# Performance work log

Measured on AMD Instinct MI355X. Metric: run time of the kernel, lower is better.

The kernel has to match this reference:

```python
import jax, jax.numpy as jnp
import numpy as np

L, NH, H, V, MAXP = 12, 12, 768, 50257, 1024
HD = H // NH
EPS = 1e-5


def setup_inputs() -> dict:
    key = jax.random.key(0)
    ks = iter(jax.random.split(key, 32))
    s = 0.02
    inp = {
        "input_ids": jax.random.randint(next(ks), (8, 1024), 0, V),
        "tok_emb": jax.random.normal(next(ks), (V, H), jnp.float32) * s,
        "pos_emb": jax.random.normal(next(ks), (MAXP, H), jnp.float32) * s,
        "ln1_g": jnp.ones((L, H), jnp.float32),
        "ln1_b": jnp.zeros((L, H), jnp.float32),
        "w_attn": jax.random.normal(next(ks), (L, H, 3 * H), jnp.float32) * s,
        "b_attn": jnp.zeros((L, 3 * H), jnp.float32),
        "w_out": jax.random.normal(next(ks), (L, H, H), jnp.float32) * s,
        "b_out": jnp.zeros((L, H), jnp.float32),
        "ln2_g": jnp.ones((L, H), jnp.float32),
        "ln2_b": jnp.zeros((L, H), jnp.float32),
        "w1": jax.random.normal(next(ks), (L, H, 4 * H), jnp.float32) * s,
        "b1": jnp.zeros((L, 4 * H), jnp.float32),
        "w2": jax.random.normal(next(ks), (L, 4 * H, H), jnp.float32) * s,
        "b2": jnp.zeros((L, H), jnp.float32),
        "lnf_g": jnp.ones((H,), jnp.float32),
        "lnf_b": jnp.zeros((H,), jnp.float32),
    }
    return inp


def _ln(x, g, b):
    mu = jnp.mean(x, axis=-1, keepdims=True)
    var = jnp.var(x, axis=-1, keepdims=True)
    return (x - mu) * jax.lax.rsqrt(var + EPS) * g + b


def _gpt2_forward(input_ids, tok_emb, pos_emb, ln1_g, ln1_b, w_attn, b_attn,
                  w_out, b_out, ln2_g, ln2_b, w1, b1, w2, b2, lnf_g, lnf_b):
    B, S = input_ids.shape
    x = tok_emb[input_ids] + pos_emb[:S]  # [B,S,H]
    # causal mask: True above the diagonal (future positions)
    mask = jnp.triu(jnp.ones((S, S), dtype=bool), k=1)
    inv_sqrt_hd = 1.0 / np.sqrt(HD)
    for l in range(L):
        n1 = _ln(x, ln1_g[l], ln1_b[l])
        qkv = n1 @ w_attn[l] + b_attn[l]  # [B,S,3H]
        q, k, v = jnp.split(qkv, 3, axis=-1)
        q = q.reshape(B, S, NH, HD).transpose(0, 2, 1, 3)
        k = k.reshape(B, S, NH, HD).transpose(0, 2, 1, 3)
        v = v.reshape(B, S, NH, HD).transpose(0, 2, 1, 3)
        scores = jnp.einsum('bhtd,bhsd->bhts', q, k)  # [B,NH,S,S]
        # faithful to source: mask with -10000 BEFORE dividing by sqrt(head_size)
        scores = jnp.where(mask, -10000.0, scores) * inv_sqrt_hd
        probs = jax.nn.softmax(scores, axis=-1)
        attn = jnp.einsum('bhts,bhsd->bhtd', probs, v)
        attn = attn.transpose(0, 2, 1, 3).reshape(B, S, H)
        attn = attn @ w_out[l] + b_out[l]
        x = x + attn
        n2 = _ln(x, ln2_g[l], ln2_b[l])
        h = jax.nn.gelu(n2 @ w1[l] + b1[l], approximate=False)
        x = x + (h @ w2[l] + b2[l])
    x = _ln(x, lnf_g, lnf_b)
    final_encoding = x[:, -1]  # [B,H]
    logits = final_encoding @ tok_emb.T  # tied weights, [B,V]
    return logits, final_encoding


def reference(input_ids, tok_emb, pos_emb, ln1_g, ln1_b, w_attn, b_attn,
              w_out, b_out, ln2_g, ln2_b, w1, b1, w2, b2, lnf_g, lnf_b):
    return _gpt2_forward(input_ids, tok_emb, pos_emb, ln1_g, ln1_b, w_attn,
                         b_attn, w_out, b_out, ln2_g, ln2_b, w1, b1, w2, b2,
                         lnf_g, lnf_b)
```

## Files before the change

kernel.cpp:

```cpp
#include <hip/hip_runtime.h>
#include <cmath>

typedef unsigned short u16;
typedef __bf16 bf16;
typedef __attribute__((ext_vector_type(8))) bf16 bf16x8;
typedef __attribute__((ext_vector_type(4))) float f32x4;

#define DINL __device__ __forceinline__

#define BB 8
#define SS 1024
#define HH 768
#define LL 12
#define NHH 12
#define HDD 64
#define MM 8192
#define VV 50257

DINL u16 f2bf(float f) {
    unsigned int u = __builtin_bit_cast(unsigned int, f);
    u += 0x7fff + ((u >> 16) & 1);
    return (u16)(u >> 16);
}

DINL bf16x8 ld_bf8(const u16* p) { return *(const bf16x8*)p; }

typedef __attribute__((address_space(1))) unsigned int as1_u32;
typedef __attribute__((address_space(3))) unsigned int as3_u32;

DINL void gllds16(const void* g, void* l) {
    __builtin_amdgcn_global_load_lds((as1_u32*)g, (as3_u32*)l, 16, 0, 0);
}

DINL void xcd_remap(int gx, int& mTile, int& nTile) {
    int i = blockIdx.y * gx + blockIdx.x;
    int xcd = i & 7, j = i >> 3;
    nTile = j % gx;
    mTile = (j / gx) * 8 + xcd;
}

__global__ __launch_bounds__(256) void k_embed(const int* __restrict__ ids,
                                               const float* __restrict__ tok,
                                               const float* __restrict__ pos,
                                               float* __restrict__ x) {
    int tk = blockIdx.x;
    int s = tk & (SS - 1);
    int id = ids[tk];
    const float* tr = tok + (size_t)id * HH;
    const float* pr = pos + (size_t)s * HH;
    float* xr = x + (size_t)tk * HH;
#pragma unroll
    for (int j = 0; j < 3; j++) {
        int d = threadIdx.x + j * 256;
        xr[d] = tr[d] + pr[d];
    }
}

__global__ __launch_bounds__(256) void k_tcvt(const float* __restrict__ src, u16* __restrict__ dst,
                                              int R, int C, size_t sstr, size_t dstr) {
    src += (size_t)blockIdx.z * sstr;
    dst += (size_t)blockIdx.z * dstr;
    __shared__ float t[32][33];
    int tx = threadIdx.x & 31, ty = threadIdx.x >> 5;
    int c0 = blockIdx.x * 32, r0 = blockIdx.y * 32;
#pragma unroll
    for (int p = 0; p < 4; p++)
        t[ty + p * 8][tx] = src[(size_t)(r0 + ty + p * 8) * C + c0 + tx];
    __syncthreads();
#pragma unroll
    for (int p = 0; p < 4; p++)
        dst[(size_t)(c0 + ty + p * 8) * R + r0 + tx] = f2bf(t[tx][ty + p * 8]);
}

template <bool F32OUT>
__global__ __launch_bounds__(256) void k_ln(const float* __restrict__ x, const float* __restrict__ g,
                                            const float* __restrict__ b, void* __restrict__ outp,
                                            int nrows, int rs, int ro) {
    int w = threadIdx.x >> 6, lane = threadIdx.x & 63;
    int row = blockIdx.x * 4 + w;
    if (row >= nrows) return;
    const float4* xr = (const float4*)(x + ((size_t)row * rs + ro) * HH);
    float4 v[3];
    float s = 0.f, s2 = 0.f;
#pragma unroll
    for (int j = 0; j < 3; j++) {
        v[j] = xr[lane + 64 * j];
        s += v[j].x + v[j].y + v[j].z + v[j].w;
        s2 += v[j].x * v[j].x + v[j].y * v[j].y + v[j].z * v[j].z + v[j].w * v[j].w;
    }
#pragma unroll
    for (int off = 32; off; off >>= 1) {
        s += __shfl_xor(s, off, 64);
        s2 += __shfl_xor(s2, off, 64);
    }
    float mu = s * (1.0f / HH);
    float rstd = rsqrtf(s2 * (1.0f / HH) - mu * mu + 1e-5f);
#pragma unroll
    for (int j = 0; j < 3; j++) {
        int d4 = lane + 64 * j;
        float4 gv = ((const float4*)g)[d4];
        float4 bv = ((const float4*)b)[d4];
        float o0 = (v[j].x - mu) * rstd * gv.x + bv.x;
        float o1 = (v[j].y - mu) * rstd * gv.y + bv.y;
        float o2 = (v[j].z - mu) * rstd * gv.z + bv.z;
        float o3 = (v[j].w - mu) * rstd * gv.w + bv.w;
        if (F32OUT) {
            ((float4*)outp)[(size_t)row * (HH / 4) + d4] = make_float4(o0, o1, o2, o3);
        } else {
            ushort4 pk;
            pk.x = f2bf(o0); pk.y = f2bf(o1); pk.z = f2bf(o2); pk.w = f2bf(o3);
            *(ushort4*)((u16*)outp + (size_t)row * HH + d4 * 4) = pk;
        }
    }
}

template <int EPI>
__global__ __launch_bounds__(256) void k_gemm(const u16* __restrict__ A, const u16* __restrict__ BT,
                                              const float* __restrict__ bias, float* __restrict__ xio,
                                              u16* __restrict__ obuf, u16* __restrict__ qb,
                                              u16* __restrict__ kb, u16* __restrict__ vb,
                                              int N, int K) {
    __shared__ u16 As[2][128 * 32];
    __shared__ u16 Bs[2][128 * 32];
    const int t = threadIdx.x, w = t >> 6, lane = t & 63;
    const int l15 = lane & 15, l4 = lane >> 4;
    const int wr = w >> 1, wc = w & 1;
    int mT, nT;
    xcd_remap(gridDim.x, mT, nT);
    const int m0 = mT * 128, n0 = nT * 128;
    const int KT = K >> 5;

    f32x4 acc[4][4] = {};

    auto stage = [&](int buf, int kt) {
#pragma unroll
        for (int i = 0; i < 2; i++) {
            int idx = w * 2 + i;
            int row = idx * 16 + (lane >> 2);
            int kc = kt * 32 + (((lane & 3) ^ ((lane >> 3) & 3)) * 8);
            gllds16(A + (size_t)(m0 + row) * K + kc, &As[buf][idx * 512]);
            gllds16(BT + (size_t)(n0 + row) * K + kc, &Bs[buf][idx * 512]);
        }
    };

    stage(0, 0);
    __syncthreads();
    int buf = 0;
    const int sw = (l15 >> 1) & 3;
    for (int kt = 0; kt < KT; ++kt) {
        if (kt + 1 < KT) stage(buf ^ 1, kt + 1);
        bf16x8 af[4], bfr[4];
#pragma unroll
        for (int i = 0; i < 4; i++) af[i] = ld_bf8(&As[buf][(wr * 64 + i * 16 + l15) * 32 + ((l4 ^ sw) * 8)]);
#pragma unroll
        for (int j = 0; j < 4; j++) bfr[j] = ld_bf8(&Bs[buf][(wc * 64 + j * 16 + l15) * 32 + ((l4 ^ sw) * 8)]);
#pragma unroll
        for (int i = 0; i < 4; i++)
#pragma unroll
            for (int j = 0; j < 4; j++)
                acc[i][j] = __builtin_amdgcn_mfma_f32_16x16x32_bf16(af[i], bfr[j], acc[i][j], 0, 0, 0);
        __syncthreads();
        buf ^= 1;
    }

#pragma unroll
    for (int i = 0; i < 4; i++) {
#pragma unroll
        for (int j = 0; j < 4; j++) {
#pragma unroll
            for (int r = 0; r < 4; r++) {
                int row = m0 + wr * 64 + i * 16 + l4 * 4 + r;
                int n = n0 + wc * 64 + j * 16 + l15;
                float v = acc[i][j][r] + bias[n];
                if (EPI == 0) {
                    int seg = n / HH, wi = n % HH;
                    int h = wi >> 6, d = wi & 63;
                    int bi = row >> 10, s = row & (SS - 1);
                    size_t bh = (size_t)(bi * NHH + h);
                    if (seg == 0)
                        qb[(bh * SS + s) * HDD + d] = f2bf(v);
                    else if (seg == 1)
                        kb[(bh * SS + s) * HDD + d] = f2bf(v);
                    else
                        vb[(bh * HDD + d) * SS + s] = f2bf(v);
                } else if (EPI == 1) {
                    xio[(size_t)row * N + n] += v;
                } else {
                    float gl = 0.5f * v * (1.0f + erff(v * 0.70710678118654752f));
                    obuf[(size_t)row * N + n] = f2bf(gl);
                }
            }
        }
    }
}

__global__ __launch_bounds__(256) void k_gemm64(const u16* __restrict__ A, const u16* __restrict__ BT,
                                                const float* __restrict__ bias, float* __restrict__ xio,
                                                int N, int K) {
    __shared__ u16 As[2][128 * 32];
    __shared__ u16 Bs[2][64 * 32];
    const int t = threadIdx.x, w = t >> 6, lane = t & 63;
    const int l15 = lane & 15, l4 = lane >> 4;
    const int wr = w >> 1, wc = w & 1;
    int mT, nT;
    xcd_remap(gridDim.x, mT, nT);
    const int m0 = mT * 128, n0 = nT * 64;
    const int KT = K >> 5;

    f32x4 acc[4][2] = {};

    auto stage = [&](int buf, int kt) {
        int rr = lane >> 2;
        int kc = kt * 32 + (((lane & 3) ^ ((lane >> 3) & 3)) * 8);
#pragma unroll
        for (int i = 0; i < 2; i++) {
            int idx = w * 2 + i;
            gllds16(A + (size_t)(m0 + idx * 16 + rr) * K + kc, &As[buf][idx * 512]);
        }
        gllds16(BT + (size_t)(n0 + w * 16 + rr) * K + kc, &Bs[buf][w * 512]);
    };

    stage(0, 0);
    __syncthreads();
    int buf = 0;
    const int sw = (l15 >> 1) & 3;
    for (int kt = 0; kt < KT; ++kt) {
        if (kt + 1 < KT) stage(buf ^ 1, kt + 1);
        bf16x8 af[4], bfr[2];
#pragma unroll
        for (int i = 0; i < 4; i++) af[i] = ld_bf8(&As[buf][(wr * 64 + i * 16 + l15) * 32 + ((l4 ^ sw) * 8)]);
#pragma unroll
        for (int j = 0; j < 2; j++) bfr[j] = ld_bf8(&Bs[buf][(wc * 32 + j * 16 + l15) * 32 + ((l4 ^ sw) * 8)]);
#pragma unroll
        for (int i = 0; i < 4; i++)
#pragma unroll
            for (int j = 0; j < 2; j++)
                acc[i][j] = __builtin_amdgcn_mfma_f32_16x16x32_bf16(af[i], bfr[j], acc[i][j], 0, 0, 0);
        __syncthreads();
        buf ^= 1;
    }

#pragma unroll
    for (int i = 0; i < 4; i++) {
#pragma unroll
        for (int j = 0; j < 2; j++) {
#pragma unroll
            for (int r = 0; r < 4; r++) {
                int row = m0 + wr * 64 + i * 16 + l4 * 4 + r;
                int n = n0 + wc * 32 + j * 16 + l15;
                xio[(size_t)row * N + n] += acc[i][j][r] + bias[n];
            }
        }
    }
}

__global__ __launch_bounds__(256) void k_attn(const u16* __restrict__ q, const u16* __restrict__ k,
                                              const u16* __restrict__ vt, u16* __restrict__ o) {
    int qt = 15 - blockIdx.x;
    int bh = blockIdx.y;
    int w = threadIdx.x >> 6, lane = threadIdx.x & 63;
    int l15 = lane & 15, l4 = lane >> 4;

    __shared__ u16 Ks[2][64 * 64];
    __shared__ u16 Vs[2][64 * 64];
    __shared__ u16 pl[4][16 * 72];
    u16* pw = pl[w];

    const size_t bhq = (size_t)bh * SS * HDD;
    int qrow0 = qt * 64 + w * 16;

    auto stage = [&](int buf, int kvb) {
#pragma unroll
        for (int i = 0; i < 2; i++) {
            int rl = w * 16 + i * 8 + (lane >> 3);
            int c = lane & 7;
            int sc = (c ^ (rl & 7)) * 8;
            gllds16(k + bhq + (size_t)(kvb * 64 + rl) * HDD + sc, &Ks[buf][(w * 16 + i * 8) * 64]);
            gllds16(vt + ((size_t)bh * HDD + rl) * SS + kvb * 64 + sc, &Vs[buf][(w * 16 + i * 8) * 64]);
        }
    };

    bf16x8 aq[2];
#pragma unroll
    for (int ks = 0; ks < 2; ks++)
        aq[ks] = ld_bf8(q + bhq + (size_t)(qrow0 + l15) * HDD + ks * 32 + l4 * 8);

    f32x4 acc[4] = {};
    float mrun[4], psum[4];
#pragma unroll
    for (int r = 0; r < 4; r++) { mrun[r] = -1e30f; psum[r] = 0.f; }

    stage(0, 0);
    __syncthreads();
    int buf = 0;

    for (int kvb = 0; kvb <= qt; ++kvb) {
        if (kvb < qt) stage(buf ^ 1, kvb + 1);

        f32x4 s[4] = {};
#pragma unroll
        for (int c = 0; c < 4; c++) {
#pragma unroll
            for (int ks = 0; ks < 2; ks++) {
                bf16x8 kf = ld_bf8(&Ks[buf][(c * 16 + l15) * 64 + ((ks * 4 + l4) ^ (l15 & 7)) * 8]);
                s[c] = __builtin_amdgcn_mfma_f32_16x16x32_bf16(aq[ks], kf, s[c], 0, 0, 0);
            }
        }
        bool diag = (kvb == qt);
#pragma unroll
        for (int c = 0; c < 4; c++) {
#pragma unroll
            for (int r = 0; r < 4; r++) {
                float val = s[c][r] * 0.125f;
                if (diag) {
                    int kvi = kvb * 64 + c * 16 + l15;
                    int qi = qrow0 + l4 * 4 + r;
                    if (kvi > qi) val = -1250.0f;
                }
                s[c][r] = val;
            }
        }
        float lmax[4];
#pragma unroll
        for (int r = 0; r < 4; r++)
            lmax[r] = fmaxf(fmaxf(s[0][r], s[1][r]), fmaxf(s[2][r], s[3][r]));
        int ok = 1;
#pragma unroll
        for (int r = 0; r < 4; r++) ok &= (lmax[r] <= mrun[r] + 8.f) ? 1 : 0;
        if (!__all(ok)) {
#pragma unroll
            for (int off = 1; off < 16; off <<= 1)
#pragma unroll
                for (int r = 0; r < 4; r++) lmax[r] = fmaxf(lmax[r], __shfl_xor(lmax[r], off, 64));
#pragma unroll
            for (int r = 0; r < 4; r++) {
                float mnew = fmaxf(mrun[r], lmax[r]);
                float ef = __expf(mrun[r] - mnew);
                mrun[r] = mnew;
                psum[r] *= ef;
#pragma unroll
                for (int cd = 0; cd < 4; cd++) acc[cd][r] *= ef;
            }
        }
#pragma unroll
        for (int c = 0; c < 4; c++)
#pragma unroll
            for (int r = 0; r < 4; r++) {
                float pv = __expf(s[c][r] - mrun[r]);
                psum[r] += pv;
                pw[(l4 * 4 + r) * 72 + c * 16 + l15] = f2bf(pv);
            }
#pragma unroll
        for (int ks = 0; ks < 2; ks++) {
            bf16x8 pa = ld_bf8(pw + l15 * 72 + ks * 32 + l4 * 8);
#pragma unroll
            for (int cd = 0; cd < 4; cd++) {
                bf16x8 vf = ld_bf8(&Vs[buf][(cd * 16 + l15) * 64 + ((ks * 4 + l4) ^ (l15 & 7)) * 8]);
                acc[cd] = __builtin_amdgcn_mfma_f32_16x16x32_bf16(pa, vf, acc[cd], 0, 0, 0);
            }
        }
        __syncthreads();
        buf ^= 1;
    }

#pragma unroll
    for (int off = 1; off < 16; off <<= 1)
#pragma unroll
        for (int r = 0; r < 4; r++) psum[r] += __shfl_xor(psum[r], off, 64);

    int b = bh / NHH, h = bh % NHH;
#pragma unroll
    for (int cd = 0; cd < 4; cd++) {
#pragma unroll
        for (int r = 0; r < 4; r++) {
            int qi = qrow0 + l4 * 4 + r;
            float ov = acc[cd][r] / psum[r];
            o[((size_t)b * SS + qi) * HH + h * HDD + cd * 16 + l15] = f2bf(ov);
        }
    }
}

__global__ __launch_bounds__(256) void k_logits(const float* __restrict__ enc,
                                                const float* __restrict__ tok,
                                                float* __restrict__ out) {
    int w = threadIdx.x >> 6, lane = threadIdx.x & 63;
    int v = blockIdx.x * 4 + w;
    if (v >= VV) return;
    const float4* tr = (const float4*)(tok + (size_t)v * HH);
    float a[8];
#pragma unroll
    for (int b = 0; b < 8; b++) a[b] = 0.f;
#pragma unroll
    for (int j = 0; j < 3; j++) {
        float4 t4 = tr[lane + 64 * j];
#pragma unroll
        for (int b = 0; b < 8; b++) {
            float4 e4 = *(const float4*)(enc + (size_t)b * HH + (lane + 64 * j) * 4);
            a[b] += t4.x * e4.x + t4.y * e4.y + t4.z * e4.z + t4.w * e4.w;
        }
    }
#pragma unroll
    for (int off = 32; off; off >>= 1)
#pragma unroll
        for (int b = 0; b < 8; b++) a[b] += __shfl_xor(a[b], off, 64);
    if (lane == 0) {
#pragma unroll
        for (int b = 0; b < 8; b++) out[(size_t)b * VV + v] = a[b];
    }
}

extern "C" void kernel_launch(void* const* d_in, const int* in_sizes, int n_in,
                              void* d_out, int out_size, void* d_ws, size_t ws_size,
                              hipStream_t stream) {
    const int* ids = (const int*)d_in[0];
    const float* tok = (const float*)d_in[1];
    const float* pos = (const float*)d_in[2];
    const float* ln1g = (const float*)d_in[3];
    const float* ln1b = (const float*)d_in[4];
    const float* wat = (const float*)d_in[5];
    const float* bat = (const float*)d_in[6];
    const float* wou = (const float*)d_in[7];
    const float* bou = (const float*)d_in[8];
    const float* ln2g = (const float*)d_in[9];
    const float* ln2b = (const float*)d_in[10];
    const float* w1 = (const float*)d_in[11];
    const float* b1 = (const float*)d_in[12];
    const float* w2 = (const float*)d_in[13];
    const float* b2 = (const float*)d_in[14];
    const float* lnfg = (const float*)d_in[15];
    const float* lnfb = (const float*)d_in[16];

    char* ws = (char*)d_ws;
    float* xw = (float*)(ws + 0);
    u16* nb = (u16*)(ws + 25165824);
    u16* qb = (u16*)(ws + 37748736);
    u16* kb = (u16*)(ws + 50331648);
    u16* vb = (u16*)(ws + 62914560);
    u16* ab = (u16*)(ws + 75497472);
    u16* hb = (u16*)(ws + 88080384);
    u16* wt = (u16*)(ws + 138412032);
    const size_t LSTR = 7077888;
    const size_t WAO = 0, WOO = 1769472, W1O = 2359296, W2O = 4718592;

    float* outf = (float*)d_out;
    float* enc = outf + (size_t)BB * VV;

    k_embed<<<MM, 256, 0, stream>>>(ids, tok, pos, xw);
    k_tcvt<<<dim3(72, 24, 12), 256, 0, stream>>>(wat, wt + WAO, 768, 2304, (size_t)768 * 2304, LSTR);
    k_tcvt<<<dim3(24, 24, 12), 256, 0, stream>>>(wou, wt + WOO, 768, 768, (size_t)768 * 768, LSTR);
    k_tcvt<<<dim3(96, 24, 12), 256, 0, stream>>>(w1, wt + W1O, 768, 3072, (size_t)768 * 3072, LSTR);
    k_tcvt<<<dim3(24, 96, 12), 256, 0, stream>>>(w2, wt + W2O, 3072, 768, (size_t)3072 * 768, LSTR);

    for (int l = 0; l < LL; l++) {
        const u16* wl = wt + (size_t)l * LSTR;
        k_ln<false><<<MM / 4, 256, 0, stream>>>(xw, ln1g + l * HH, ln1b + l * HH, nb, MM, 1, 0);
        k_gemm<0><<<dim3(18, 64), 256, 0, stream>>>(nb, wl + WAO, bat + (size_t)l * 2304,
                                                    nullptr, nullptr, qb, kb, vb, 2304, 768);
        k_attn<<<dim3(16, 96), 256, 0, stream>>>(qb, kb, vb, ab);
        k_gemm64<<<dim3(12, 64), 256, 0, stream>>>(ab, wl + WOO, bou + (size_t)l * HH, xw, 768, 768);
        k_ln<false><<<MM / 4, 256, 0, stream>>>(xw, ln2g + l * HH, ln2b + l * HH, nb, MM, 1, 0);
        k_gemm<2><<<dim3(24, 64), 256, 0, stream>>>(nb, wl + W1O, b1 + (size_t)l * 3072,
                                                    nullptr, hb, nullptr, nullptr, nullptr, 3072, 768);
        k_gemm64<<<dim3(12, 64), 256, 0, stream>>>(hb, wl + W2O, b2 + (size_t)l * HH, xw, 768, 3072);
    }
    k_ln<true><<<2, 256, 0, stream>>>(xw, lnfg, lnfb, enc, BB, SS, SS - 1);
    k_logits<<<(VV + 3) / 4, 256, 0, stream>>>(enc, tok, outf);
}
```

Baseline: 3.899 ms.

## Enlarge attention query tile to 128 rows and fold softmax scale into Q

The attention kernel now processes 128 query rows per block (32 per wave, two MFMA row groups), so each staged K/V tile in shared memory feeds twice as many queries and the grid halves. Waves skip KV blocks beyond their own causal limit, and the 1/sqrt(head_dim) scale moves into the QKV GEMM epilogue so the per-score multiply goes away. In exchange there is higher register pressure and fewer blocks (768 vs 1536), which may reduce occupancy and worsen causal load imbalance. Scaling Q before the bf16 cast also slightly changes rounding.

```diff
diff --git a/kernel.cpp b/kernel.cpp
--- a/kernel.cpp
+++ b/kernel.cpp
@@ -178,7 +178,7 @@
                     int bi = row >> 10, s = row & (SS - 1);
                     size_t bh = (size_t)(bi * NHH + h);
                     if (seg == 0)
-                        qb[(bh * SS + s) * HDD + d] = f2bf(v);
+                        qb[(bh * SS + s) * HDD + d] = f2bf(v * 0.125f);
                     else if (seg == 1)
                         kb[(bh * SS + s) * HDD + d] = f2bf(v);
                     else
@@ -256,18 +256,20 @@
 
 __global__ __launch_bounds__(256) void k_attn(const u16* __restrict__ q, const u16* __restrict__ k,
                                               const u16* __restrict__ vt, u16* __restrict__ o) {
-    int qt = 15 - blockIdx.x;
+    int qt = 7 - blockIdx.x;
     int bh = blockIdx.y;
     int w = threadIdx.x >> 6, lane = threadIdx.x & 63;
     int l15 = lane & 15, l4 = lane >> 4;
 
     __shared__ u16 Ks[2][64 * 64];
     __shared__ u16 Vs[2][64 * 64];
-    __shared__ u16 pl[4][16 * 72];
+    __shared__ u16 pl[4][32 * 72];
     u16* pw = pl[w];
 
     const size_t bhq = (size_t)bh * SS * HDD;
-    int qrow0 = qt * 64 + w * 16;
+    const int qrow0 = qt * 128 + w * 32;
+    const int nfull = qrow0 >> 6;
+    const int kvmax = 2 * qt + 1;
 
     auto stage = [&](int buf, int kvb) {
 #pragma unroll
@@ -280,83 +282,104 @@
         }
     };
 
-    bf16x8 aq[2];
-#pragma unroll
-    for (int ks = 0; ks < 2; ks++)
-        aq[ks] = ld_bf8(q + bhq + (size_t)(qrow0 + l15) * HDD + ks * 32 + l4 * 8);
-
-    f32x4 acc[4] = {};
-    float mrun[4], psum[4];
-#pragma unroll
-    for (int r = 0; r < 4; r++) { mrun[r] = -1e30f; psum[r] = 0.f; }
+    bf16x8 aq[2][2];
+#pragma unroll
+    for (int m = 0; m < 2; m++)
+#pragma unroll
+        for (int ks = 0; ks < 2; ks++)
+            aq[m][ks] = ld_bf8(q + bhq + (size_t)(qrow0 + m * 16 + l15) * HDD + ks * 32 + l4 * 8);
+
+    f32x4 acc[2][4] = {};
+    float mrun[2][4], psum[2][4];
+#pragma unroll
+    for (int m = 0; m < 2; m++)
+#pragma unroll
+        for (int r = 0; r < 4; r++) { mrun[m][r] = -1e30f; psum[m][r] = 0.f; }
 
     stage(0, 0);
     __syncthreads();
     int buf = 0;
 
-    for (int kvb = 0; kvb <= qt; ++kvb) {
-        if (kvb < qt) stage(buf ^ 1, kvb + 1);
-
-        f32x4 s[4] = {};
-#pragma unroll
-        for (int c = 0; c < 4; c++) {
+    for (int kvb = 0; kvb <= kvmax; ++kvb) {
+        if (kvb < kvmax) stage(buf ^ 1, kvb + 1);
+
+        if (kvb <= nfull) {
+            f32x4 s[2][4] = {};
+#pragma unroll
+            for (int c = 0; c < 4; c++) {
+#pragma unroll
+                for (int ks = 0; ks < 2; ks++) {
+                    bf16x8 kf = ld_bf8(&Ks[buf][(c * 16 + l15) * 64 + ((ks * 4 + l4) ^ (l15 & 7)) * 8]);
+#pragma unroll
+                    for (int m = 0; m < 2; m++)
+                        s[m][c] = __builtin_amdgcn_mfma_f32_16x16x32_bf16(aq[m][ks], kf, s[m][c], 0, 0, 0);
+                }
+            }
+            if (kvb == nfull) {
+#pragma unroll
+                for (int c = 0; c < 4; c++) {
+                    int kvi = kvb * 64 + c * 16 + l15;
+#pragma unroll
+                    for (int m = 0; m < 2; m++)
+#pragma unroll
+                        for (int r = 0; r < 4; r++) {
+                            int qi = qrow0 + m * 16 + l4 * 4 + r;
+                            if (kvi > qi) s[m][c][r] = -1250.0f;
+                        }
+                }
+            }
+            float lmax[2][4];
+            int ok = 1;
+#pragma unroll
+            for (int m = 0; m < 2; m++)
+#pragma unroll
+                for (int r = 0; r < 4; r++) {
+                    lmax[m][r] = fmaxf(fmaxf(s[m][0][r], s[m][1][r]), fmaxf(s[m][2][r], s[m][3][r]));
+                    ok &= (lmax[m][r] <= mrun[m][r] + 8.f) ? 1 : 0;
+                }
+            if (!__all(ok)) {
+#pragma unroll
+                for (int off = 1; off < 16; off <<= 1)
+#pragma unroll
+                    for (int m = 0; m < 2; m++)
+#pragma unroll
+                        for (int r = 0; r < 4; r++)
+                            lmax[m][r] = fmaxf(lmax[m][r], __shfl_xor(lmax[m][r], off, 64));
+#pragma unroll
+                for (int m = 0; m < 2; m++)
+#pragma unroll
+                    for (int r = 0; r < 4; r++) {
+                        float mnew = fmaxf(mrun[m][r], lmax[m][r]);
+                        float ef = __expf(mrun[m][r] - mnew);
+                        mrun[m][r] = mnew;
+                        psum[m][r] *= ef;
+#pragma unroll
+                        for (int cd = 0; cd < 4; cd++) acc[m][cd][r] *= ef;
+                    }
+            }
+#pragma unroll
+            for (int c = 0; c < 4; c++)
+#pragma unroll
+                for (int m = 0; m < 2; m++)
+#pragma unroll
+                    for (int r = 0; r < 4; r++) {
+                        float pv = __expf(s[m][c][r] - mrun[m][r]);
+                        psum[m][r] += pv;
+                        pw[(m * 16 + l4 * 4 + r) * 72 + c * 16 + l15] = f2bf(pv);
+                    }
 #pragma unroll
             for (int ks = 0; ks < 2; ks++) {
-                bf16x8 kf = ld_bf8(&Ks[buf][(c * 16 + l15) * 64 + ((ks * 4 + l4) ^ (l15 & 7)) * 8]);
-                s[c] = __builtin_amdgcn_mfma_f32_16x16x32_bf16(aq[ks], kf, s[c], 0, 0, 0);
-            }
-        }
-        bool diag = (kvb == qt);
-#pragma unroll
-        for (int c = 0; c < 4; c++) {
-#pragma unroll
-            for (int r = 0; r < 4; r++) {
-                float val = s[c][r] * 0.125f;
-                if (diag) {
-                    int kvi = kvb * 64 + c * 16 + l15;
-                    int qi = qrow0 + l4 * 4 + r;
-                    if (kvi > qi) val = -1250.0f;
+                bf16x8 pa[2];
+#pragma unroll
+                for (int m = 0; m < 2; m++)
+                    pa[m] = ld_bf8(pw + (m * 16 + l15) * 72 + ks * 32 + l4 * 8);
+#pragma unroll
+                for (int cd = 0; cd < 4; cd++) {
+                    bf16x8 vf = ld_bf8(&Vs[buf][(cd * 16 + l15) * 64 + ((ks * 4 + l4) ^ (l15 & 7)) * 8]);
+#pragma unroll
+                    for (int m = 0; m < 2; m++)
+                        acc[m][cd] = __builtin_amdgcn_mfma_f32_16x16x32_bf16(pa[m], vf, acc[m][cd], 0, 0, 0);
                 }
-                s[c][r] = val;
-            }
-        }
-        float lmax[4];
-#pragma unroll
-        for (int r = 0; r < 4; r++)
-            lmax[r] = fmaxf(fmaxf(s[0][r], s[1][r]), fmaxf(s[2][r], s[3][r]));
-        int ok = 1;
-#pragma unroll
-        for (int r = 0; r < 4; r++) ok &= (lmax[r] <= mrun[r] + 8.f) ? 1 : 0;
-        if (!__all(ok)) {
-#pragma unroll
-            for (int off = 1; off < 16; off <<= 1)
-#pragma unroll
-                for (int r = 0; r < 4; r++) lmax[r] = fmaxf(lmax[r], __shfl_xor(lmax[r], off, 64));
-#pragma unroll
-            for (int r = 0; r < 4; r++) {
-                float mnew = fmaxf(mrun[r], lmax[r]);
-                float ef = __expf(mrun[r] - mnew);
-                mrun[r] = mnew;
-                psum[r] *= ef;
-#pragma unroll
-                for (int cd = 0; cd < 4; cd++) acc[cd][r] *= ef;
-            }
-        }
-#pragma unroll
-        for (int c = 0; c < 4; c++)
-#pragma unroll
-            for (int r = 0; r < 4; r++) {
-                float pv = __expf(s[c][r] - mrun[r]);
-                psum[r] += pv;
-                pw[(l4 * 4 + r) * 72 + c * 16 + l15] = f2bf(pv);
-            }
-#pragma unroll
-        for (int ks = 0; ks < 2; ks++) {
-            bf16x8 pa = ld_bf8(pw + l15 * 72 + ks * 32 + l4 * 8);
-#pragma unroll
-            for (int cd = 0; cd < 4; cd++) {
-                bf16x8 vf = ld_bf8(&Vs[buf][(cd * 16 + l15) * 64 + ((ks * 4 + l4) ^ (l15 & 7)) * 8]);
-                acc[cd] = __builtin_amdgcn_mfma_f32_16x16x32_bf16(pa, vf, acc[cd], 0, 0, 0);
             }
         }
         __syncthreads();
@@ -366,18 +389,22 @@
 #pragma unroll
     for (int off = 1; off < 16; off <<= 1)
 #pragma unroll
-        for (int r = 0; r < 4; r++) psum[r] += __shfl_xor(psum[r], off, 64);
+        for (int m = 0; m < 2; m++)
+#pragma unroll
+            for (int r = 0; r < 4; r++) psum[m][r] += __shfl_xor(psum[m][r], off, 64);
 
     int b = bh / NHH, h = bh % NHH;
 #pragma unroll
-    for (int cd = 0; cd < 4; cd++) {
-#pragma unroll
-        for (int r = 0; r < 4; r++) {
-            int qi = qrow0 + l4 * 4 + r;
-            float ov = acc[cd][r] / psum[r];
-            o[((size_t)b * SS + qi) * HH + h * HDD + cd * 16 + l15] = f2bf(ov);
-        }
-    }
+    for (int m = 0; m < 2; m++)
+#pragma unroll
+        for (int cd = 0; cd < 4; cd++) {
+#pragma unroll
+            for (int r = 0; r < 4; r++) {
+                int qi = qrow0 + m * 16 + l4 * 4 + r;
+                float ov = acc[m][cd][r] / psum[m][r];
+                o[((size_t)b * SS + qi) * HH + h * HDD + cd * 16 + l15] = f2bf(ov);
+            }
+        }
 }
 
 __global__ __launch_bounds__(256) void k_logits(const float* __restrict__ enc,
@@ -456,7 +483,7 @@
         k_ln<false><<<MM / 4, 256, 0, stream>>>(xw, ln1g + l * HH, ln1b + l * HH, nb, MM, 1, 0);
         k_gemm<0><<<dim3(18, 64), 256, 0, stream>>>(nb, wl + WAO, bat + (size_t)l * 2304,
                                                     nullptr, nullptr, qb, kb, vb, 2304, 768);
-        k_attn<<<dim3(16, 96), 256, 0, stream>>>(qb, kb, vb, ab);
+        k_attn<<<dim3(8, 96), 256, 0, stream>>>(qb, kb, vb, ab);
         k_gemm64<<<dim3(12, 64), 256, 0, stream>>>(ab, wl + WOO, bou + (size_t)l * HH, xw, 768, 768);
         k_ln<false><<<MM / 4, 256, 0, stream>>>(xw, ln2g + l * HH, ln2b + l * HH, nb, MM, 1, 0);
         k_gemm<2><<<dim3(24, 64), 256, 0, stream>>>(nb, wl + W1O, b1 + (size_t)l * 3072,
```

After: 4.058 ms. 1.04x slower.

## Replace 128x128 GEMM with 256x256 eight-wave pipelined GEMM for QKV and FC1

Applied to the files above, without the earlier changes.

Swaps the 128x128 bf16 GEMM used for the QKV and FC1 projections for a 512-thread kernel with 256x256 tiles, K-step 64, and 128KB of dynamic LDS. Staging is split into half-tiles with explicit vmcnt waits, raw barriers and s_setprio around the MFMA blocks, so global-to-LDS loads overlap compute and reuse per load goes up. The 1/sqrt(hd) scale moves into the Q store in the GEMM epilogue and the attention kernel drops the per-element multiply. The cost is fewer blocks per grid (288/384) and heavy register and LDS use, which limits occupancy, plus a fragile hand-written wait schedule.

```diff
diff --git a/kernel.cpp b/kernel.cpp
--- a/kernel.cpp
+++ b/kernel.cpp
@@ -31,6 +31,13 @@
 DINL void gllds16(const void* g, void* l) {
     __builtin_amdgcn_global_load_lds((as1_u32*)g, (as3_u32*)l, 16, 0, 0);
 }
+
+#define BARRIER()                                   \
+    do {                                            \
+        asm volatile("" ::: "memory");              \
+        __builtin_amdgcn_s_barrier();               \
+        asm volatile("" ::: "memory");              \
+    } while (0)
 
 DINL void xcd_remap(int gx, int& mTile, int& nTile) {
     int i = blockIdx.y * gx + blockIdx.x;
@@ -115,76 +122,145 @@
 }
 
 template <int EPI>
-__global__ __launch_bounds__(256) void k_gemm(const u16* __restrict__ A, const u16* __restrict__ BT,
-                                              const float* __restrict__ bias, float* __restrict__ xio,
-                                              u16* __restrict__ obuf, u16* __restrict__ qb,
-                                              u16* __restrict__ kb, u16* __restrict__ vb,
-                                              int N, int K) {
-    __shared__ u16 As[2][128 * 32];
-    __shared__ u16 Bs[2][128 * 32];
+__global__ __launch_bounds__(512, 2) void k_gemm256(const u16* __restrict__ A, const u16* __restrict__ BT,
+                                                    const float* __restrict__ bias,
+                                                    u16* __restrict__ obuf, u16* __restrict__ qb,
+                                                    u16* __restrict__ kb, u16* __restrict__ vb,
+                                                    int N, int K) {
+    extern __shared__ u16 LD[];
     const int t = threadIdx.x, w = t >> 6, lane = t & 63;
     const int l15 = lane & 15, l4 = lane >> 4;
-    const int wr = w >> 1, wc = w & 1;
+    const int wm = w >> 2, wn = w & 3;
     int mT, nT;
     xcd_remap(gridDim.x, mT, nT);
-    const int m0 = mT * 128, n0 = nT * 128;
-    const int KT = K >> 5;
-
-    f32x4 acc[4][4] = {};
-
-    auto stage = [&](int buf, int kt) {
+    const int m0 = mT * 256, n0 = nT * 256;
+    const int KT = K >> 6, NI = KT >> 1;
+
+    auto seg = [&](int buf, int mat, int h) -> u16* {
+        return LD + (size_t)(((buf * 2 + mat) * 2 + h) * 8192);
+    };
+
+    auto stageH = [&](int buf, int mat, int h, int kt) {
+        const u16* src = mat ? BT : A;
+        const int base0 = mat ? n0 : m0;
+        u16* dst = seg(buf, mat, h);
 #pragma unroll
         for (int i = 0; i < 2; i++) {
-            int idx = w * 2 + i;
-            int row = idx * 16 + (lane >> 2);
-            int kc = kt * 32 + (((lane & 3) ^ ((lane >> 3) & 3)) * 8);
-            gllds16(A + (size_t)(m0 + row) * K + kc, &As[buf][idx * 512]);
-            gllds16(BT + (size_t)(n0 + row) * K + kc, &Bs[buf][idx * 512]);
+            int rl = w * 16 + i * 8 + (lane >> 3);
+            int c = lane & 7;
+            int sc = (c ^ (rl & 7)) * 8;
+            gllds16(src + (size_t)(base0 + h * 128 + rl) * K + kt * 64 + sc,
+                    dst + (w * 16 + i * 8) * 64);
         }
     };
 
-    stage(0, 0);
-    __syncthreads();
-    int buf = 0;
-    const int sw = (l15 >> 1) & 3;
-    for (int kt = 0; kt < KT; ++kt) {
-        if (kt + 1 < KT) stage(buf ^ 1, kt + 1);
-        bf16x8 af[4], bfr[4];
-#pragma unroll
-        for (int i = 0; i < 4; i++) af[i] = ld_bf8(&As[buf][(wr * 64 + i * 16 + l15) * 32 + ((l4 ^ sw) * 8)]);
-#pragma unroll
-        for (int j = 0; j < 4; j++) bfr[j] = ld_bf8(&Bs[buf][(wc * 64 + j * 16 + l15) * 32 + ((l4 ^ sw) * 8)]);
-#pragma unroll
-        for (int i = 0; i < 4; i++)
-#pragma unroll
-            for (int j = 0; j < 4; j++)
-                acc[i][j] = __builtin_amdgcn_mfma_f32_16x16x32_bf16(af[i], bfr[j], acc[i][j], 0, 0, 0);
-        __syncthreads();
-        buf ^= 1;
-    }
-
-#pragma unroll
-    for (int i = 0; i < 4; i++) {
-#pragma unroll
-        for (int j = 0; j < 4; j++) {
+    f32x4 acc[8][4] = {};
+    const int csw = l15 & 7;
+
+    auto rdA = [&](int buf, int mh, bf16x8 a[4][2]) {
+        const u16* p = seg(buf, 0, wm);
+#pragma unroll
+        for (int f = 0; f < 4; f++)
+#pragma unroll
+            for (int s = 0; s < 2; s++)
+                a[f][s] = ld_bf8(p + (mh * 64 + f * 16 + l15) * 64 + ((s * 4 + l4) ^ csw) * 8);
+    };
+    auto rdB = [&](int buf, bf16x8 b[4][2]) {
+        const u16* p = seg(buf, 1, wn >> 1);
+#pragma unroll
+        for (int f = 0; f < 4; f++)
+#pragma unroll
+            for (int s = 0; s < 2; s++)
+                b[f][s] = ld_bf8(p + ((wn & 1) * 64 + f * 16 + l15) * 64 + ((s * 4 + l4) ^ csw) * 8);
+    };
+
+    stageH(0, 0, 0, 0); stageH(0, 0, 1, 0);
+    stageH(0, 1, 0, 0); stageH(0, 1, 1, 0);
+    stageH(1, 1, 0, 1); stageH(1, 1, 1, 1);
+    asm volatile("s_waitcnt vmcnt(4)" ::: "memory");
+    BARRIER();
+
+    for (int i = 0; i < NI; ++i) {
+        const int tE = 2 * i, tO = 2 * i + 1;
+        const bool lst = (i == NI - 1);
+        bf16x8 a[4][2], b[4][2];
+
+        rdA(0, 0, a); rdB(0, b);
+        stageH(1, 0, 0, tO); stageH(1, 0, 1, tO);
+        __builtin_amdgcn_s_setprio(1);
+#pragma unroll
+        for (int f = 0; f < 4; f++)
+#pragma unroll
+            for (int nf = 0; nf < 4; nf++)
+#pragma unroll
+                for (int s = 0; s < 2; s++)
+                    acc[f][nf] = __builtin_amdgcn_mfma_f32_16x16x32_bf16(a[f][s], b[nf][s], acc[f][nf], 0, 0, 0);
+        __builtin_amdgcn_s_setprio(0);
+        BARRIER();
+
+        rdA(0, 1, a);
+        if (!lst) { stageH(0, 1, 0, tE + 2); stageH(0, 1, 1, tE + 2); }
+        __builtin_amdgcn_s_setprio(1);
+#pragma unroll
+        for (int f = 0; f < 4; f++)
+#pragma unroll
+            for (int nf = 0; nf < 4; nf++)
+#pragma unroll
+                for (int s = 0; s < 2; s++)
+                    acc[4 + f][nf] = __builtin_amdgcn_mfma_f32_16x16x32_bf16(a[f][s], b[nf][s], acc[4 + f][nf], 0, 0, 0);
+        __builtin_amdgcn_s_setprio(0);
+        if (lst) asm volatile("s_waitcnt vmcnt(0)" ::: "memory");
+        else     asm volatile("s_waitcnt vmcnt(4)" ::: "memory");
+        BARRIER();
+
+        rdA(1, 0, a); rdB(1, b);
+        if (!lst) { stageH(0, 0, 0, tE + 2); stageH(0, 0, 1, tE + 2); }
+        __builtin_amdgcn_s_setprio(1);
+#pragma unroll
+        for (int f = 0; f < 4; f++)
+#pragma unroll
+            for (int nf = 0; nf < 4; nf++)
+#pragma unroll
+                for (int s = 0; s < 2; s++)
+                    acc[f][nf] = __builtin_amdgcn_mfma_f32_16x16x32_bf16(a[f][s], b[nf][s], acc[f][nf], 0, 0, 0);
+        __builtin_amdgcn_s_setprio(0);
+        BARRIER();
+
+        rdA(1, 1, a);
+        if (!lst) { stageH(1, 1, 0, tO + 2); stageH(1, 1, 1, tO + 2); }
+        __builtin_amdgcn_s_setprio(1);
+#pragma unroll
+        for (int f = 0; f < 4; f++)
+#pragma unroll
+            for (int nf = 0; nf < 4; nf++)
+#pragma unroll
+                for (int s = 0; s < 2; s++)
+                    acc[4 + f][nf] = __builtin_amdgcn_mfma_f32_16x16x32_bf16(a[f][s], b[nf][s], acc[4 + f][nf], 0, 0, 0);
+        __builtin_amdgcn_s_setprio(0);
+        if (!lst) asm volatile("s_waitcnt vmcnt(4)" ::: "memory");
+        BARRIER();
+    }
+
+#pragma unroll
+    for (int mf = 0; mf < 8; mf++) {
+#pragma unroll
+        for (int nf = 0; nf < 4; nf++) {
 #pragma unroll
             for (int r = 0; r < 4; r++) {
-                int row = m0 + wr * 64 + i * 16 + l4 * 4 + r;
-                int n = n0 + wc * 64 + j * 16 + l15;
-                float v = acc[i][j][r] + bias[n];
+                int row = m0 + wm * 128 + mf * 16 + l4 * 4 + r;
+                int n = n0 + wn * 64 + nf * 16 + l15;
+                float v = acc[mf][nf][r] + bias[n];
                 if (EPI == 0) {
-                    int seg = n / HH, wi = n % HH;
+                    int sg = n / HH, wi = n % HH;
                     int h = wi >> 6, d = wi & 63;
                     int bi = row >> 10, s = row & (SS - 1);
                     size_t bh = (size_t)(bi * NHH + h);
-                    if (seg == 0)
-                        qb[(bh * SS + s) * HDD + d] = f2bf(v);
-                    else if (seg == 1)
+                    if (sg == 0)
+                        qb[(bh * SS + s) * HDD + d] = f2bf(v * 0.125f);
+                    else if (sg == 1)
                         kb[(bh * SS + s) * HDD + d] = f2bf(v);
                     else
                         vb[(bh * HDD + d) * SS + s] = f2bf(v);
-                } else if (EPI == 1) {
-                    xio[(size_t)row * N + n] += v;
                 } else {
                     float gl = 0.5f * v * (1.0f + erff(v * 0.70710678118654752f));
                     obuf[(size_t)row * N + n] = f2bf(gl);
@@ -306,27 +382,24 @@
                 s[c] = __builtin_amdgcn_mfma_f32_16x16x32_bf16(aq[ks], kf, s[c], 0, 0, 0);
             }
         }
-        bool diag = (kvb == qt);
-#pragma unroll
-        for (int c = 0; c < 4; c++) {
-#pragma unroll
-            for (int r = 0; r < 4; r++) {
-                float val = s[c][r] * 0.125f;
-                if (diag) {
-                    int kvi = kvb * 64 + c * 16 + l15;
+        if (kvb == qt) {
+#pragma unroll
+            for (int c = 0; c < 4; c++) {
+                int kvi = kvb * 64 + c * 16 + l15;
+#pragma unroll
+                for (int r = 0; r < 4; r++) {
                     int qi = qrow0 + l4 * 4 + r;
-                    if (kvi > qi) val = -1250.0f;
+                    if (kvi > qi) s[c][r] = -1250.0f;
                 }
-                s[c][r] = val;
             }
         }
         float lmax[4];
-#pragma unroll
-        for (int r = 0; r < 4; r++)
+        int ok = 1;
+#pragma unroll
+        for (int r = 0; r < 4; r++) {
             lmax[r] = fmaxf(fmaxf(s[0][r], s[1][r]), fmaxf(s[2][r], s[3][r]));
-        int ok = 1;
-#pragma unroll
-        for (int r = 0; r < 4; r++) ok &= (lmax[r] <= mrun[r] + 8.f) ? 1 : 0;
+            ok &= (lmax[r] <= mrun[r] + 8.f) ? 1 : 0;
+        }
         if (!__all(ok)) {
 #pragma unroll
             for (int off = 1; off < 16; off <<= 1)
@@ -445,6 +518,15 @@
     float* outf = (float*)d_out;
     float* enc = outf + (size_t)BB * VV;
 
+    static bool attrDone = false;
+    if (!attrDone) {
+        hipFuncSetAttribute(reinterpret_cast<const void*>(&k_gemm256<0>),
+                            hipFuncAttributeMaxDynamicSharedMemorySize, 131072);
+        hipFuncSetAttribute(reinterpret_cast<const void*>(&k_gemm256<2>),
+                            hipFuncAttributeMaxDynamicSharedMemorySize, 131072);
+        attrDone = true;
+    }
+
     k_embed<<<MM, 256, 0, stream>>>(ids, tok, pos, xw);
     k_tcvt<<<dim3(72, 24, 12), 256, 0, stream>>>(wat, wt + WAO, 768, 2304, (size_t)768 * 2304, LSTR);
     k_tcvt<<<dim3(24, 24, 12), 256, 0, stream>>>(wou, wt + WOO, 768, 768, (size_t)768 * 768, LSTR);
@@ -454,13 +536,13 @@
     for (int l = 0; l < LL; l++) {
         const u16* wl = wt + (size_t)l * LSTR;
         k_ln<false><<<MM / 4, 256, 0, stream>>>(xw, ln1g + l * HH, ln1b + l * HH, nb, MM, 1, 0);
-        k_gemm<0><<<dim3(18, 64), 256, 0, stream>>>(nb, wl + WAO, bat + (size_t)l * 2304,
-                                                    nullptr, nullptr, qb, kb, vb, 2304, 768);
+        k_gemm256<0><<<dim3(9, 32), 512, 131072, stream>>>(nb, wl + WAO, bat + (size_t)l * 2304,
+                                                           nullptr, qb, kb, vb, 2304, 768);
         k_attn<<<dim3(16, 96), 256, 0, stream>>>(qb, kb, vb, ab);
         k_gemm64<<<dim3(12, 64), 256, 0, stream>>>(ab, wl + WOO, bou + (size_t)l * HH, xw, 768, 768);
         k_ln<false><<<MM / 4, 256, 0, stream>>>(xw, ln2g + l * HH, ln2b + l * HH, nb, MM, 1, 0);
-        k_gemm<2><<<dim3(24, 64), 256, 0, stream>>>(nb, wl + W1O, b1 + (size_t)l * 3072,
-                                                    nullptr, hb, nullptr, nullptr, nullptr, 3072, 768);
+        k_gemm256<2><<<dim3(12, 32), 512, 131072, stream>>>(nb, wl + W1O, b1 + (size_t)l * 3072,
+                                                            hb, nullptr, nullptr, nullptr, 3072, 768);
         k_gemm64<<<dim3(12, 64), 256, 0, stream>>>(hb, wl + W2O, b2 + (size_t)l * HH, xw, 768, 3072);
     }
     k_ln<true><<<2, 256, 0, stream>>>(xw, lnfg, lnfb, enc, BB, SS, SS - 1);
```

After: 4.065 ms. 4.2% more time.

## Triple-buffer GEMM LDS staging with explicit vmcnt waits and fold attention scale into Q

Applied to the files above, without the earlier changes.

Both GEMM kernels move from double to triple-buffered LDS staging. Tiles are prefetched two steps ahead, with explicit s_waitcnt vmcnt counts and raw s_barrier in place of __syncthreads, and MFMA sections are wrapped in s_setprio. This aims to hide global-to-LDS load latency better and cut stalls at each k-step. Separately, the 1/sqrt(64) scale is folded into the Q write of the QKV epilogue so attention skips a per-element multiply. That fold changes bf16 rounding slightly, and the LDS footprint grows, which may lower occupancy.

```diff
diff --git a/kernel.cpp b/kernel.cpp
--- a/kernel.cpp
+++ b/kernel.cpp
@@ -31,6 +31,13 @@
 DINL void gllds16(const void* g, void* l) {
     __builtin_amdgcn_global_load_lds((as1_u32*)g, (as3_u32*)l, 16, 0, 0);
 }
+
+#define BARRIER()                                   \
+    do {                                            \
+        asm volatile("" ::: "memory");              \
+        __builtin_amdgcn_s_barrier();               \
+        asm volatile("" ::: "memory");              \
+    } while (0)
 
 DINL void xcd_remap(int gx, int& mTile, int& nTile) {
     int i = blockIdx.y * gx + blockIdx.x;
@@ -116,12 +123,12 @@
 
 template <int EPI>
 __global__ __launch_bounds__(256) void k_gemm(const u16* __restrict__ A, const u16* __restrict__ BT,
-                                              const float* __restrict__ bias, float* __restrict__ xio,
+                                              const float* __restrict__ bias,
                                               u16* __restrict__ obuf, u16* __restrict__ qb,
                                               u16* __restrict__ kb, u16* __restrict__ vb,
                                               int N, int K) {
-    __shared__ u16 As[2][128 * 32];
-    __shared__ u16 Bs[2][128 * 32];
+    __shared__ u16 As[3][128 * 32];
+    __shared__ u16 Bs[3][128 * 32];
     const int t = threadIdx.x, w = t >> 6, lane = t & 63;
     const int l15 = lane & 15, l4 = lane >> 4;
     const int wr = w >> 1, wc = w & 1;
@@ -144,23 +151,36 @@
     };
 
     stage(0, 0);
-    __syncthreads();
-    int buf = 0;
+    if (KT > 1) stage(1, 1);
     const int sw = (l15 >> 1) & 3;
+
     for (int kt = 0; kt < KT; ++kt) {
-        if (kt + 1 < KT) stage(buf ^ 1, kt + 1);
+        int nb = kt + 2;
+        if (nb < KT) {
+            stage(nb % 3, nb);
+            asm volatile("s_waitcnt vmcnt(8)" ::: "memory");
+        } else if (kt + 1 < KT) {
+            asm volatile("s_waitcnt vmcnt(4)" ::: "memory");
+        } else {
+            asm volatile("s_waitcnt vmcnt(0)" ::: "memory");
+        }
+        BARRIER();
+
+        const u16* ap = As[kt % 3];
+        const u16* bp = Bs[kt % 3];
         bf16x8 af[4], bfr[4];
 #pragma unroll
-        for (int i = 0; i < 4; i++) af[i] = ld_bf8(&As[buf][(wr * 64 + i * 16 + l15) * 32 + ((l4 ^ sw) * 8)]);
-#pragma unroll
-        for (int j = 0; j < 4; j++) bfr[j] = ld_bf8(&Bs[buf][(wc * 64 + j * 16 + l15) * 32 + ((l4 ^ sw) * 8)]);
+        for (int i = 0; i < 4; i++) af[i] = ld_bf8(ap + (wr * 64 + i * 16 + l15) * 32 + ((l4 ^ sw) * 8));
+#pragma unroll
+        for (int j = 0; j < 4; j++) bfr[j] = ld_bf8(bp + (wc * 64 + j * 16 + l15) * 32 + ((l4 ^ sw) * 8));
+        __builtin_amdgcn_s_setprio(1);
 #pragma unroll
         for (int i = 0; i < 4; i++)
 #pragma unroll
             for (int j = 0; j < 4; j++)
                 acc[i][j] = __builtin_amdgcn_mfma_f32_16x16x32_bf16(af[i], bfr[j], acc[i][j], 0, 0, 0);
-        __syncthreads();
-        buf ^= 1;
+        __builtin_amdgcn_s_setprio(0);
+        BARRIER();
     }
 
 #pragma unroll
@@ -173,18 +193,16 @@
                 int n = n0 + wc * 64 + j * 16 + l15;
                 float v = acc[i][j][r] + bias[n];
                 if (EPI == 0) {
-                    int seg = n / HH, wi = n % HH;
+                    int sg = n / HH, wi = n % HH;
                     int h = wi >> 6, d = wi & 63;
                     int bi = row >> 10, s = row & (SS - 1);
                     size_t bh = (size_t)(bi * NHH + h);
-                    if (seg == 0)
-                        qb[(bh * SS + s) * HDD + d] = f2bf(v);
-                    else if (seg == 1)
+                    if (sg == 0)
+                        qb[(bh * SS + s) * HDD + d] = f2bf(v * 0.125f);
+                    else if (sg == 1)
                         kb[(bh * SS + s) * HDD + d] = f2bf(v);
                     else
                         vb[(bh * HDD + d) * SS + s] = f2bf(v);
-                } else if (EPI == 1) {
-                    xio[(size_t)row * N + n] += v;
                 } else {
                     float gl = 0.5f * v * (1.0f + erff(v * 0.70710678118654752f));
                     obuf[(size_t)row * N + n] = f2bf(gl);
@@ -197,8 +215,8 @@
 __global__ __launch_bounds__(256) void k_gemm64(const u16* __restrict__ A, const u16* __restrict__ BT,
                                                 const float* __restrict__ bias, float* __restrict__ xio,
                                                 int N, int K) {
-    __shared__ u16 As[2][128 * 32];
-    __shared__ u16 Bs[2][64 * 32];
+    __shared__ u16 As[3][128 * 32];
+    __shared__ u16 Bs[3][64 * 32];
     const int t = threadIdx.x, w = t >> 6, lane = t & 63;
     const int l15 = lane & 15, l4 = lane >> 4;
     const int wr = w >> 1, wc = w & 1;
@@ -221,23 +239,36 @@
     };
 
     stage(0, 0);
-    __syncthreads();
-    int buf = 0;
+    if (KT > 1) stage(1, 1);
     const int sw = (l15 >> 1) & 3;
+
     for (int kt = 0; kt < KT; ++kt) {
-        if (kt + 1 < KT) stage(buf ^ 1, kt + 1);
+        int nb = kt + 2;
+        if (nb < KT) {
+            stage(nb % 3, nb);
+            asm volatile("s_waitcnt vmcnt(6)" ::: "memory");
+        } else if (kt + 1 < KT) {
+            asm volatile("s_waitcnt vmcnt(3)" ::: "memory");
+        } else {
+            asm volatile("s_waitcnt vmcnt(0)" ::: "memory");
+        }
+        BARRIER();
+
+        const u16* ap = As[kt % 3];
+        const u16* bp = Bs[kt % 3];
         bf16x8 af[4], bfr[2];
 #pragma unroll
-        for (int i = 0; i < 4; i++) af[i] = ld_bf8(&As[buf][(wr * 64 + i * 16 + l15) * 32 + ((l4 ^ sw) * 8)]);
-#pragma unroll
-        for (int j = 0; j < 2; j++) bfr[j] = ld_bf8(&Bs[buf][(wc * 32 + j * 16 + l15) * 32 + ((l4 ^ sw) * 8)]);
+        for (int i = 0; i < 4; i++) af[i] = ld_bf8(ap + (wr * 64 + i * 16 + l15) * 32 + ((l4 ^ sw) * 8));
+#pragma unroll
+        for (int j = 0; j < 2; j++) bfr[j] = ld_bf8(bp + (wc * 32 + j * 16 + l15) * 32 + ((l4 ^ sw) * 8));
+        __builtin_amdgcn_s_setprio(1);
 #pragma unroll
         for (int i = 0; i < 4; i++)
 #pragma unroll
             for (int j = 0; j < 2; j++)
                 acc[i][j] = __builtin_amdgcn_mfma_f32_16x16x32_bf16(af[i], bfr[j], acc[i][j], 0, 0, 0);
-        __syncthreads();
-        buf ^= 1;
+        __builtin_amdgcn_s_setprio(0);
+        BARRIER();
     }
 
 #pragma unroll
@@ -306,27 +337,24 @@
                 s[c] = __builtin_amdgcn_mfma_f32_16x16x32_bf16(aq[ks], kf, s[c], 0, 0, 0);
             }
         }
-        bool diag = (kvb == qt);
-#pragma unroll
-        for (int c = 0; c < 4; c++) {
-#pragma unroll
-            for (int r = 0; r < 4; r++) {
-                float val = s[c][r] * 0.125f;
-                if (diag) {
-                    int kvi = kvb * 64 + c * 16 + l15;
+        if (kvb == qt) {
+#pragma unroll
+            for (int c = 0; c < 4; c++) {
+                int kvi = kvb * 64 + c * 16 + l15;
+#pragma unroll
+                for (int r = 0; r < 4; r++) {
                     int qi = qrow0 + l4 * 4 + r;
-                    if (kvi > qi) val = -1250.0f;
+                    if (kvi > qi) s[c][r] = -1250.0f;
                 }
-                s[c][r] = val;
             }
         }
         float lmax[4];
-#pragma unroll
-        for (int r = 0; r < 4; r++)
+        int ok = 1;
+#pragma unroll
+        for (int r = 0; r < 4; r++) {
             lmax[r] = fmaxf(fmaxf(s[0][r], s[1][r]), fmaxf(s[2][r], s[3][r]));
-        int ok = 1;
-#pragma unroll
-        for (int r = 0; r < 4; r++) ok &= (lmax[r] <= mrun[r] + 8.f) ? 1 : 0;
+            ok &= (lmax[r] <= mrun[r] + 8.f) ? 1 : 0;
+        }
         if (!__all(ok)) {
 #pragma unroll
             for (int off = 1; off < 16; off <<= 1)
@@ -455,12 +483,12 @@
         const u16* wl = wt + (size_t)l * LSTR;
         k_ln<false><<<MM / 4, 256, 0, stream>>>(xw, ln1g + l * HH, ln1b + l * HH, nb, MM, 1, 0);
         k_gemm<0><<<dim3(18, 64), 256, 0, stream>>>(nb, wl + WAO, bat + (size_t)l * 2304,
-                                                    nullptr, nullptr, qb, kb, vb, 2304, 768);
+                                                    nullptr, qb, kb, vb, 2304, 768);
         k_attn<<<dim3(16, 96), 256, 0, stream>>>(qb, kb, vb, ab);
         k_gemm64<<<dim3(12, 64), 256, 0, stream>>>(ab, wl + WOO, bou + (size_t)l * HH, xw, 768, 768);
         k_ln<false><<<MM / 4, 256, 0, stream>>>(xw, ln2g + l * HH, ln2b + l * HH, nb, MM, 1, 0);
         k_gemm<2><<<dim3(24, 64), 256, 0, stream>>>(nb, wl + W1O, b1 + (size_t)l * 3072,
-                                                    nullptr, hb, nullptr, nullptr, nullptr, 3072, 768);
+                                                    hb, nullptr, nullptr, nullptr, 3072, 768);
         k_gemm64<<<dim3(12, 64), 256, 0, stream>>>(hb, wl + W2O, b2 + (size_t)l * HH, xw, 768, 3072);
     }
     k_ln<true><<<2, 256, 0, stream>>>(xw, lnfg, lnfb, enc, BB, SS, SS - 1);
```

New measurement: 3.962 ms. About the same (+1.6%).
